# Optimization experiments

Hardware: AMD Instinct MI355X
Metric: run time of the kernel (lower is better)

The kernel has to match this reference:

```python
import jax, jax.numpy as jnp
import numpy as np

ATTEN = 8  # atten_size -> window W = 2*ATTEN+1 = 17


def setup_inputs() -> dict:
    key = jax.random.key(0)
    ks = jax.random.split(key, 9)
    B, S, I, H, O = 16, 4096, 64, 64, 2
    xavier = lambda k, fi, fo: jax.random.normal(k, (fi, fo), jnp.float32) * jnp.sqrt(2.0 / (fi + fo))
    return {
        "x": jax.random.normal(ks[0], (B, S, I), jnp.float32),
        "pos_enc": jax.random.normal(ks[1], (B, S, I), jnp.float32),
        "W1": xavier(ks[2], I, H),
        "b1": jnp.zeros((1, 1, H), jnp.float32),
        "Wq": xavier(ks[3], H, H),
        "Wk": xavier(ks[4], H, H),
        "Wv": xavier(ks[5], H, H),
        "W2": xavier(ks[6], H, O),
        "b2": jnp.zeros((1, 1, O), jnp.float32),
    }


def _gather_window(h, a):
    # Replicates pad + roll(k) for k in [-a, a] + stack(dim=2) + slice[a:-a]:
    # x_nei[b, t, j, :] = h[b, t + a - j, :]  (zeros when out of range)
    B, S, H = h.shape
    t = jnp.arange(S)[:, None]
    j = jnp.arange(2 * a + 1)[None, :]
    idx = t + a - j                      # [S, W]
    valid = (idx >= 0) & (idx < S)
    idxc = jnp.clip(idx, 0, S - 1)
    nei = h[:, idxc, :]                  # [B, S, W, H]
    return nei * valid[None, :, :, None].astype(h.dtype)


def reference(x, pos_enc, W1, b1, Wq, Wk, Wv, W2, b2):
    a = ATTEN
    h = x + pos_enc[: x.shape[0]]
    h = jax.nn.relu(h @ W1 + b1)                      # [B, S, H]
    H = h.shape[-1]
    x_nei = _gather_window(h, a)                      # [B, S, W, H]
    q = (h @ Wq)[:, :, None, :]                       # [B, S, 1, H]
    k = x_nei @ Wk                                    # [B, S, W, H]
    v = x_nei @ Wv                                    # [B, S, W, H]
    scores = jnp.einsum("bsoh,bswh->bsow", q, k) / jnp.sqrt(jnp.float32(H))
    # Faithful to torch.nn.Softmax(dim=2) on [B,S,1,W]: softmax over singleton dim -> all ones
    weights = jax.nn.softmax(scores, axis=2)          # [B, S, 1, W]
    att = jnp.einsum("bsow,bswh->bsoh", weights, v)[:, :, 0, :]  # [B, S, H]
    out = att @ W2 + b2                               # [B, S, O]
    return out, weights
```

## Files before the change

kernel.cpp:

```cpp
#include <hip/hip_runtime.h>
#include <hip/hip_bf16.h>

#define NS 4096
#define NTOK 65536
#define TOKB 128
#define GRID 512
#define NLOC 144
#define NTILE 9
#define WTS_V 278528u
#define F4MAX 1048575

typedef __attribute__((ext_vector_type(8))) short bfrag;
typedef __attribute__((ext_vector_type(4))) float f32x4;

__global__ __launch_bounds__(256, 2) void fused(
    const float* __restrict__ x, const float* __restrict__ pe,
    const float* __restrict__ w1p, const float* __restrict__ b1p,
    const float* __restrict__ wvp, const float* __restrict__ w2p,
    const float* __restrict__ b2p,
    float* __restrict__ out, float* __restrict__ wts)
{
    __shared__ bfrag Xb[NLOC * 8];
    __shared__ bfrag Wf[512];
    __shared__ float B1s[64], M0s[64], M1s[64];
    __shared__ float PL[146][2];

    const int tid  = threadIdx.x;
    const int blk  = blockIdx.x;
    const int lane = tid & 63;
    const int wid  = tid >> 6;

    const int gbase4 = blk * 2048 - 128;
    const float4* x4 = (const float4*)x;
    const float4* p4 = (const float4*)pe;
    #pragma unroll
    for (int it = 0; it < 5; ++it) {
        int cidx = it * 256 + tid;
        if (cidx < NLOC * 8) {
            int f0 = gbase4 + cidx * 2, f1 = f0 + 1;
            f0 = f0 < 0 ? 0 : (f0 > F4MAX ? F4MAX : f0);
            f1 = f1 < 0 ? 0 : (f1 > F4MAX ? F4MAX : f1);
            float4 a = x4[f0], b = x4[f1], c = p4[f0], d = p4[f1];
            union { __hip_bfloat162 h[4]; bfrag v; } P;
            P.h[0] = __float22bfloat162_rn(make_float2(a.x + c.x, a.y + c.y));
            P.h[1] = __float22bfloat162_rn(make_float2(a.z + c.z, a.w + c.w));
            P.h[2] = __float22bfloat162_rn(make_float2(b.x + d.x, b.y + d.y));
            P.h[3] = __float22bfloat162_rn(make_float2(b.z + d.z, b.w + d.w));
            int tl = cidx >> 3;
            int sc = (cidx & 7) ^ (tl & 7);
            Xb[tl * 8 + sc] = P.v;
        }
    }

    #pragma unroll
    for (int s = 0; s < 2; ++s) {
        int slot = s * 256 + tid;
        int kh = slot >> 8, rem = slot & 255, dt = rem >> 6, l = rem & 63;
        int dd = dt * 16 + (l & 15);
        int kb = kh * 32 + ((l >> 4) << 3);
        union { __hip_bfloat162 h[4]; bfrag v; } P;
        #pragma unroll
        for (int j = 0; j < 4; ++j) {
            float lo = w1p[(kb + 2*j)     * 64 + dd];
            float hi = w1p[(kb + 2*j + 1) * 64 + dd];
            P.h[j] = __float22bfloat162_rn(make_float2(lo, hi));
        }
        Wf[slot] = P.v;
    }
    if (tid >= 192) B1s[tid - 192] = b1p[tid - 192];

    if (tid < 128) {
        const int o = tid & 1, dd = tid >> 1;
        const float4* wv4 = (const float4*)(wvp + (size_t)dd * 64);
        const float2* w22 = (const float2*)w2p;
        float m0 = 0.f, m1 = 0.f, m2 = 0.f, m3 = 0.f;
        #pragma unroll
        for (int q = 0; q < 16; q += 4) {
            float4 a = wv4[q], b = wv4[q+1], c = wv4[q+2], e = wv4[q+3];
            #pragma unroll
            for (int r = 0; r < 4; ++r) {
                float2 u = w22[4*q + r];      float wa = o ? u.y : u.x;
                float2 v = w22[4*q + 4 + r];  float wb = o ? v.y : v.x;
                float2 w = w22[4*q + 8 + r];  float wc = o ? w.y : w.x;
                float2 z = w22[4*q + 12 + r]; float we = o ? z.y : z.x;
                float av = r == 0 ? a.x : r == 1 ? a.y : r == 2 ? a.z : a.w;
                float bv = r == 0 ? b.x : r == 1 ? b.y : r == 2 ? b.z : b.w;
                float cv = r == 0 ? c.x : r == 1 ? c.y : r == 2 ? c.z : c.w;
                float ev = r == 0 ? e.x : r == 1 ? e.y : r == 2 ? e.z : e.w;
                m0 = fmaf(av, wa, m0);
                m1 = fmaf(bv, wb, m1);
                m2 = fmaf(cv, wc, m2);
                m3 = fmaf(ev, we, m3);
            }
        }
        float v = (m0 + m1) + (m2 + m3);
        if (o) M1s[dd] = v; else M0s[dd] = v;
    }
    __syncthreads();

    const int cl = lane & 15;
    float biasv[4], m0v[4], m1v[4];
    #pragma unroll
    for (int dt = 0; dt < 4; ++dt) {
        biasv[dt] = B1s[dt * 16 + cl];
        m0v[dt]   = M0s[dt * 16 + cl];
        m1v[dt]   = M1s[dt * 16 + cl];
    }
    const int sbase = (blk & 31) * TOKB - 8;
    for (int tau = wid; tau < NTILE; tau += 4) {
        float pr0[4] = {0.f,0.f,0.f,0.f}, pr1[4] = {0.f,0.f,0.f,0.f};
        const int arow = (tau * 16 + cl) * 8;
        #pragma unroll
        for (int dt = 0; dt < 4; ++dt) {
            f32x4 acc = {0.f, 0.f, 0.f, 0.f};
            #pragma unroll
            for (int kh = 0; kh < 2; ++kh) {
                bfrag av = Xb[arow + (((kh << 2) + (lane >> 4)) ^ (lane & 7))];
                bfrag bv = Wf[(kh * 4 + dt) * 64 + lane];
                acc = __builtin_amdgcn_mfma_f32_16x16x32_bf16(av, bv, acc, 0, 0, 0);
            }
            #pragma unroll
            for (int rg = 0; rg < 4; ++rg) {
                float h = fmaxf(acc[rg] + biasv[dt], 0.f);
                pr0[rg] = fmaf(h, m0v[dt], pr0[rg]);
                pr1[rg] = fmaf(h, m1v[dt], pr1[rg]);
            }
        }
        #pragma unroll
        for (int rg = 0; rg < 4; ++rg) {
            #pragma unroll
            for (int m = 1; m < 16; m <<= 1) {
                pr0[rg] += __shfl_xor(pr0[rg], m);
                pr1[rg] += __shfl_xor(pr1[rg], m);
            }
        }
        if ((lane & 15) == 0) {
            const int rgrp = lane >> 4;
            #pragma unroll
            for (int rg = 0; rg < 4; ++rg) {
                int tl = tau * 16 + rgrp * 4 + rg;
                bool valid = (unsigned)(sbase + tl) < (unsigned)NS;
                PL[tl][0] = valid ? pr0[rg] : 0.f;
                PL[tl][1] = valid ? pr1[rg] : 0.f;
            }
        }
    }

    {
        float4* wp = (float4*)wts;
        const float4 one4 = make_float4(1.f, 1.f, 1.f, 1.f);
        for (unsigned idx = (unsigned)blk * 256u + (unsigned)tid;
             idx < WTS_V; idx += (unsigned)GRID * 256u)
            wp[idx] = one4;
    }
    __syncthreads();

    if (tid < TOKB) {
        float ax = b2p[0], ay = b2p[1];
        #pragma unroll
        for (int k = 0; k <= 16; ++k) {
            float2 v = *(const float2*)&PL[tid + k][0];
            ax += v.x; ay += v.y;
        }
        ((float2*)out)[(size_t)blk * TOKB + tid] = make_float2(ax, ay);
    }
}

extern "C" void kernel_launch(void* const* d_in, const int* in_sizes, int n_in,
                              void* d_out, int out_size, void* d_ws, size_t ws_size,
                              hipStream_t stream) {
    const float* x  = (const float*)d_in[0];
    const float* pe = (const float*)d_in[1];
    const float* w1 = (const float*)d_in[2];
    const float* b1 = (const float*)d_in[3];
    const float* wv = (const float*)d_in[6];
    const float* w2 = (const float*)d_in[7];
    const float* b2 = (const float*)d_in[8];

    float* out = (float*)d_out;
    float* wts = out + (size_t)NTOK * 2;

    fused<<<GRID, 256, 0, stream>>>(x, pe, w1, b1, wv, w2, b2, out, wts);
}
```

Measured before the change: 93.64 us.

## Load x+pe directly into MFMA A-fragments in registers, prefetch next tile

Removes the shared-memory staging buffer for the x+pos_enc tile. Each lane now loads its own A-operand float4s straight from global memory into registers, and the first two tiles are issued before the weight and bias setup so the loads overlap it. The third tile's load is issued between compute steps. This drops LDS writes and reads plus their bank-swizzle logic, at the cost of more register pressure and less coalesced global loads, since each lane reads 2×32B per row.

```diff
diff --git a/kernel.cpp b/kernel.cpp
--- a/kernel.cpp
+++ b/kernel.cpp
@@ -5,13 +5,71 @@
 #define NTOK 65536
 #define TOKB 128
 #define GRID 512
-#define NLOC 144
 #define NTILE 9
 #define WTS_V 278528u
-#define F4MAX 1048575
 
 typedef __attribute__((ext_vector_type(8))) short bfrag;
 typedef __attribute__((ext_vector_type(4))) float f32x4;
+
+#define ISSUE_TILE(XB, PB, TAU)                                         \
+    {                                                                   \
+        int g_ = blk * TOKB - 8 + (TAU) * 16 + cl;                      \
+        g_ = g_ < 0 ? 0 : (g_ > NTOK - 1 ? NTOK - 1 : g_);              \
+        const float4* xa_ = x4 + (size_t)g_ * 16 + kq * 2;              \
+        const float4* pa_ = p4 + (size_t)g_ * 16 + kq * 2;              \
+        XB[0] = xa_[0]; XB[1] = xa_[1];                       \
+        XB[2] = xa_[8]; XB[3] = xa_[9];                       \
+        PB[0] = pa_[0]; PB[1] = pa_[1];                                 \
+        PB[2] = pa_[8]; PB[3] = pa_[9];                                 \
+    }
+
+__device__ __forceinline__ void compute_tile(
+    const float4 (&xb)[4], const float4 (&pb)[4], int tau,
+    const bfrag (&Wf)[512], const float* biasv, const float* m0v,
+    const float* m1v, int lane, int sbase, float (&PL)[146][2])
+{
+    union { __hip_bfloat162 h[4]; bfrag v; } A0, A1;
+    A0.h[0] = __float22bfloat162_rn(make_float2(xb[0].x + pb[0].x, xb[0].y + pb[0].y));
+    A0.h[1] = __float22bfloat162_rn(make_float2(xb[0].z + pb[0].z, xb[0].w + pb[0].w));
+    A0.h[2] = __float22bfloat162_rn(make_float2(xb[1].x + pb[1].x, xb[1].y + pb[1].y));
+    A0.h[3] = __float22bfloat162_rn(make_float2(xb[1].z + pb[1].z, xb[1].w + pb[1].w));
+    A1.h[0] = __float22bfloat162_rn(make_float2(xb[2].x + pb[2].x, xb[2].y + pb[2].y));
+    A1.h[1] = __float22bfloat162_rn(make_float2(xb[2].z + pb[2].z, xb[2].w + pb[2].w));
+    A1.h[2] = __float22bfloat162_rn(make_float2(xb[3].x + pb[3].x, xb[3].y + pb[3].y));
+    A1.h[3] = __float22bfloat162_rn(make_float2(xb[3].z + pb[3].z, xb[3].w + pb[3].w));
+
+    float pr0[4] = {0.f,0.f,0.f,0.f}, pr1[4] = {0.f,0.f,0.f,0.f};
+    #pragma unroll
+    for (int dt = 0; dt < 4; ++dt) {
+        f32x4 acc = {0.f, 0.f, 0.f, 0.f};
+        acc = __builtin_amdgcn_mfma_f32_16x16x32_bf16(A0.v, Wf[dt * 64 + lane], acc, 0, 0, 0);
+        acc = __builtin_amdgcn_mfma_f32_16x16x32_bf16(A1.v, Wf[(4 + dt) * 64 + lane], acc, 0, 0, 0);
+        #pragma unroll
+        for (int rg = 0; rg < 4; ++rg) {
+            float h = fmaxf(acc[rg] + biasv[dt], 0.f);
+            pr0[rg] = fmaf(h, m0v[dt], pr0[rg]);
+            pr1[rg] = fmaf(h, m1v[dt], pr1[rg]);
+        }
+    }
+    #pragma unroll
+    for (int rg = 0; rg < 4; ++rg) {
+        #pragma unroll
+        for (int m = 1; m < 16; m <<= 1) {
+            pr0[rg] += __shfl_xor(pr0[rg], m);
+            pr1[rg] += __shfl_xor(pr1[rg], m);
+        }
+    }
+    if ((lane & 15) == 0) {
+        const int rgrp = lane >> 4;
+        #pragma unroll
+        for (int rg = 0; rg < 4; ++rg) {
+            int tl = tau * 16 + rgrp * 4 + rg;
+            bool valid = (unsigned)(sbase + tl) < (unsigned)NS;
+            PL[tl][0] = valid ? pr0[rg] : 0.f;
+            PL[tl][1] = valid ? pr1[rg] : 0.f;
+        }
+    }
+}
 
 __global__ __launch_bounds__(256, 2) void fused(
     const float* __restrict__ x, const float* __restrict__ pe,
@@ -20,7 +78,6 @@
     const float* __restrict__ b2p,
     float* __restrict__ out, float* __restrict__ wts)
 {
-    __shared__ bfrag Xb[NLOC * 8];
     __shared__ bfrag Wf[512];
     __shared__ float B1s[64], M0s[64], M1s[64];
     __shared__ float PL[146][2];
@@ -29,28 +86,17 @@
     const int blk  = blockIdx.x;
     const int lane = tid & 63;
     const int wid  = tid >> 6;
+    const int cl   = lane & 15;
+    const int kq   = lane >> 4;
 
-    const int gbase4 = blk * 2048 - 128;
     const float4* x4 = (const float4*)x;
     const float4* p4 = (const float4*)pe;
-    #pragma unroll
-    for (int it = 0; it < 5; ++it) {
-        int cidx = it * 256 + tid;
-        if (cidx < NLOC * 8) {
-            int f0 = gbase4 + cidx * 2, f1 = f0 + 1;
-            f0 = f0 < 0 ? 0 : (f0 > F4MAX ? F4MAX : f0);
-            f1 = f1 < 0 ? 0 : (f1 > F4MAX ? F4MAX : f1);
-            float4 a = x4[f0], b = x4[f1], c = p4[f0], d = p4[f1];
-            union { __hip_bfloat162 h[4]; bfrag v; } P;
-            P.h[0] = __float22bfloat162_rn(make_float2(a.x + c.x, a.y + c.y));
-            P.h[1] = __float22bfloat162_rn(make_float2(a.z + c.z, a.w + c.w));
-            P.h[2] = __float22bfloat162_rn(make_float2(b.x + d.x, b.y + d.y));
-            P.h[3] = __float22bfloat162_rn(make_float2(b.z + d.z, b.w + d.w));
-            int tl = cidx >> 3;
-            int sc = (cidx & 7) ^ (tl & 7);
-            Xb[tl * 8 + sc] = P.v;
-        }
-    }
+
+    const int t0 = wid, t1 = wid + 4, t2 = wid + 8;
+
+    float4 xb0[4], pb0[4], xb1[4], pb1[4];
+    ISSUE_TILE(xb0, pb0, t0);
+    ISSUE_TILE(xb1, pb1, t1);
 
     #pragma unroll
     for (int s = 0; s < 2; ++s) {
@@ -98,7 +144,6 @@
     }
     __syncthreads();
 
-    const int cl = lane & 15;
     float biasv[4], m0v[4], m1v[4];
     #pragma unroll
     for (int dt = 0; dt < 4; ++dt) {
@@ -107,44 +152,12 @@
         m1v[dt]   = M1s[dt * 16 + cl];
     }
     const int sbase = (blk & 31) * TOKB - 8;
-    for (int tau = wid; tau < NTILE; tau += 4) {
-        float pr0[4] = {0.f,0.f,0.f,0.f}, pr1[4] = {0.f,0.f,0.f,0.f};
-        const int arow = (tau * 16 + cl) * 8;
-        #pragma unroll
-        for (int dt = 0; dt < 4; ++dt) {
-            f32x4 acc = {0.f, 0.f, 0.f, 0.f};
-            #pragma unroll
-            for (int kh = 0; kh < 2; ++kh) {
-                bfrag av = Xb[arow + (((kh << 2) + (lane >> 4)) ^ (lane & 7))];
-                bfrag bv = Wf[(kh * 4 + dt) * 64 + lane];
-                acc = __builtin_amdgcn_mfma_f32_16x16x32_bf16(av, bv, acc, 0, 0, 0);
-            }
-            #pragma unroll
-            for (int rg = 0; rg < 4; ++rg) {
-                float h = fmaxf(acc[rg] + biasv[dt], 0.f);
-                pr0[rg] = fmaf(h, m0v[dt], pr0[rg]);
-                pr1[rg] = fmaf(h, m1v[dt], pr1[rg]);
-            }
-        }
-        #pragma unroll
-        for (int rg = 0; rg < 4; ++rg) {
-            #pragma unroll
-            for (int m = 1; m < 16; m <<= 1) {
-                pr0[rg] += __shfl_xor(pr0[rg], m);
-                pr1[rg] += __shfl_xor(pr1[rg], m);
-            }
-        }
-        if ((lane & 15) == 0) {
-            const int rgrp = lane >> 4;
-            #pragma unroll
-            for (int rg = 0; rg < 4; ++rg) {
-                int tl = tau * 16 + rgrp * 4 + rg;
-                bool valid = (unsigned)(sbase + tl) < (unsigned)NS;
-                PL[tl][0] = valid ? pr0[rg] : 0.f;
-                PL[tl][1] = valid ? pr1[rg] : 0.f;
-            }
-        }
-    }
+
+    compute_tile(xb0, pb0, t0, Wf, biasv, m0v, m1v, lane, sbase, PL);
+    if (t2 < NTILE) ISSUE_TILE(xb0, pb0, t2);
+    compute_tile(xb1, pb1, t1, Wf, biasv, m0v, m1v, lane, sbase, PL);
+    if (t2 < NTILE)
+        compute_tile(xb0, pb0, t2, Wf, biasv, m0v, m1v, lane, sbase, PL);
 
     {
         float4* wp = (float4*)wts;
```

Result: no change. 93.18 us (-0.5%).
